# Kernel tuning notes

Hardware: AMD Instinct MI355X
Metric: run time of the kernel (lower is better)

Reference implementation:

```python
import jax, jax.numpy as jnp
import numpy as np

NB_HEAD = 16
SIZE_PER_HEAD = 64
D_MODEL = 1024
OUT_DIM = NB_HEAD * SIZE_PER_HEAD
BIG_NEG = 1e10


def setup_inputs() -> dict:
    key = jax.random.key(0)
    ks = jax.random.split(key, 6)
    B, L = 2, 2048
    q = jax.random.normal(ks[0], (B, L, D_MODEL), dtype=jnp.float32)
    k = jax.random.normal(ks[1], (B, L, D_MODEL), dtype=jnp.float32)
    v = jax.random.normal(ks[2], (B, L, D_MODEL), dtype=jnp.float32)
    v_mask = jnp.ones((B, L), dtype=jnp.float32)
    q_mask = jnp.ones((B, L), dtype=jnp.float32)
    # glorot_normal-ish init for the three projection kernels
    std = (2.0 / (D_MODEL + OUT_DIM)) ** 0.5
    q_kernel = jax.random.normal(ks[3], (D_MODEL, OUT_DIM), dtype=jnp.float32) * std
    k_kernel = jax.random.normal(ks[4], (D_MODEL, OUT_DIM), dtype=jnp.float32) * std
    v_kernel = jax.random.normal(ks[5], (D_MODEL, OUT_DIM), dtype=jnp.float32) * std
    return {"q": q, "k": k, "v": v, "v_mask": v_mask, "q_mask": q_mask,
            "q_kernel": q_kernel, "k_kernel": k_kernel, "v_kernel": v_kernel}


def reference(q, k, v, v_mask, q_mask, q_kernel, k_kernel, v_kernel):
    B, Lq, _ = q.shape
    Lk = k.shape[1]
    H, D = NB_HEAD, SIZE_PER_HEAD
    # projections -> [B, L, H, D]
    qw = (q @ q_kernel).reshape(B, Lq, H, D)
    kw = (k @ k_kernel).reshape(B, Lk, H, D)
    vw = (v @ v_kernel).reshape(B, Lk, H, D)
    # scaled dot-product scores [B, H, Lq, Lk]
    scores = jnp.einsum('bqhd,bkhd->bhqk', qw, kw) / jnp.sqrt(jnp.float32(D))
    # additive key mask (original permutes so mask broadcasts over key axis)
    scores = scores - (1.0 - v_mask)[:, None, None, :] * BIG_NEG
    a = jax.nn.softmax(scores, axis=-1)
    # weighted sum -> [B, Lq, H, D] -> [B, Lq, H*D]
    o = jnp.einsum('bhqk,bkhd->bqhd', a, vw).reshape(B, Lq, H * D)
    # multiplicative query mask on output
    o = o * q_mask[:, :, None]
    return o
```

## Files before the change

### kernel.cpp

```cpp
#include <hip/hip_runtime.h>
#include <hip/hip_bf16.h>

#define B_SZ 2
#define SEQ  2048
#define DM   1024
#define NH   16
#define HD   64

typedef __attribute__((ext_vector_type(8))) short bf16x8;
typedef __attribute__((ext_vector_type(4))) short bf16x4;
typedef __attribute__((ext_vector_type(4))) float f32x4;

__device__ __forceinline__ short f2b(float f) {
    __hip_bfloat16 h = __float2bfloat16(f);
    return *reinterpret_cast<short*>(&h);
}

__device__ __forceinline__ void async_copy16(void* lds, const void* g) {
    __builtin_amdgcn_global_load_lds(
        (const __attribute__((address_space(1))) void*)g,
        (__attribute__((address_space(3))) void*)lds, 16, 0, 0);
}

__global__ __launch_bounds__(256) void kCvt(
    const float* __restrict__ q, const float* __restrict__ k, const float* __restrict__ v,
    short* __restrict__ qb, short* __restrict__ kb, short* __restrict__ vb) {
    const float* src = blockIdx.z == 0 ? q : (blockIdx.z == 1 ? k : v);
    short*       dst = blockIdx.z == 0 ? qb : (blockIdx.z == 1 ? kb : vb);
    size_t i = ((size_t)blockIdx.x * 256 + threadIdx.x) * 8;
    float4 a0 = *reinterpret_cast<const float4*>(src + i);
    float4 a1 = *reinterpret_cast<const float4*>(src + i + 4);
    bf16x8 c;
    c[0] = f2b(a0.x); c[1] = f2b(a0.y); c[2] = f2b(a0.z); c[3] = f2b(a0.w);
    c[4] = f2b(a1.x); c[5] = f2b(a1.y); c[6] = f2b(a1.z); c[7] = f2b(a1.w);
    *reinterpret_cast<bf16x8*>(dst + i) = c;
}

__global__ __launch_bounds__(256) void kT(
    const float* __restrict__ w0, const float* __restrict__ w1, const float* __restrict__ w2,
    short* __restrict__ t0, short* __restrict__ t1, short* __restrict__ t2) {
    const float* w = blockIdx.z == 0 ? w0 : (blockIdx.z == 1 ? w1 : w2);
    short*       t = blockIdx.z == 0 ? t0 : (blockIdx.z == 1 ? t1 : t2);
    __shared__ float tile[64][65];
    int n0 = blockIdx.x * 64, k0 = blockIdx.y * 64;
    int tid = threadIdx.x;
    int c = tid & 63, rr = tid >> 6;
#pragma unroll
    for (int i = 0; i < 16; i++) {
        int kk = i * 4 + rr;
        tile[kk][c] = w[(size_t)(k0 + kk) * DM + n0 + c];
    }
    __syncthreads();
#pragma unroll
    for (int i = 0; i < 16; i++) {
        int nn = i * 4 + rr;
        t[(size_t)(n0 + nn) * DM + k0 + c] = f2b(tile[c][nn]);
    }
}

__global__ __launch_bounds__(256) void kProj(
    const short* __restrict__ qb, const short* __restrict__ kb, const short* __restrict__ vb,
    const short* __restrict__ wtq, const short* __restrict__ wtk, const short* __restrict__ wtv,
    short* __restrict__ qw, short* __restrict__ kw, short* __restrict__ vwT) {
    int z = blockIdx.z;
    const short* A  = z == 0 ? qb : (z == 1 ? kb : vb);
    const short* Bt = z == 0 ? wtq : (z == 1 ? wtk : wtv);

    __shared__ short As[128 * 64];
    __shared__ short Bs[128 * 64];

    int tid = threadIdx.x;
    int m0 = blockIdx.y * 128, n0 = blockIdx.x * 128;
    int wv = tid >> 6, lane = tid & 63, quad = lane >> 4, ln = lane & 15;
    int rblk = (wv >> 1) * 64, cblk = (wv & 1) * 64;

    int rA = wv * 32;
    int srow = rA + (lane >> 3), scol = (lane & 7) * 8;

    f32x4 zero = {0.f, 0.f, 0.f, 0.f};
    f32x4 acc[4][4];
#pragma unroll
    for (int rt = 0; rt < 4; rt++)
#pragma unroll
        for (int ct = 0; ct < 4; ct++) acc[rt][ct] = zero;

    for (int ks = 0; ks < DM; ks += 64) {
        const short* gA = A  + (size_t)(m0 + srow) * DM + ks + scol;
        const short* gB = Bt + (size_t)(n0 + srow) * DM + ks + scol;
#pragma unroll
        for (int i = 0; i < 4; i++) {
            async_copy16(&As[(rA + i * 8) * 64], gA + (size_t)i * 8 * DM);
            async_copy16(&Bs[(rA + i * 8) * 64], gB + (size_t)i * 8 * DM);
        }
        __syncthreads();
#pragma unroll
        for (int kc = 0; kc < 2; kc++) {
            bf16x8 af[4], bfv[4];
#pragma unroll
            for (int rt = 0; rt < 4; rt++)
                af[rt] = *reinterpret_cast<bf16x8*>(&As[(rblk + rt * 16 + ln) * 64 + kc * 32 + quad * 8]);
#pragma unroll
            for (int ct = 0; ct < 4; ct++)
                bfv[ct] = *reinterpret_cast<bf16x8*>(&Bs[(cblk + ct * 16 + ln) * 64 + kc * 32 + quad * 8]);
#pragma unroll
            for (int rt = 0; rt < 4; rt++)
#pragma unroll
                for (int ct = 0; ct < 4; ct++)
                    acc[rt][ct] = __builtin_amdgcn_mfma_f32_16x16x32_bf16(
                        af[rt], bfv[ct], acc[rt][ct], 0, 0, 0);
        }
        __syncthreads();
    }

    if (z < 2) {
        short* C = z == 0 ? qw : kw;
#pragma unroll
        for (int rt = 0; rt < 4; rt++)
#pragma unroll
            for (int r = 0; r < 4; r++) {
                int row = m0 + rblk + rt * 16 + quad * 4 + r;
#pragma unroll
                for (int ct = 0; ct < 4; ct++)
                    C[(size_t)row * DM + n0 + cblk + ct * 16 + ln] = f2b(acc[rt][ct][r]);
            }
    } else {
#pragma unroll
        for (int rt = 0; rt < 4; rt++) {
            int srow0 = m0 + rblk + rt * 16 + quad * 4;
            int bb = srow0 >> 11, lk = srow0 & (SEQ - 1);
#pragma unroll
            for (int ct = 0; ct < 4; ct++) {
                int coln = n0 + cblk + ct * 16 + ln;
                int hh = coln >> 6, dd = coln & 63;
                bf16x4 pk;
                pk[0] = f2b(acc[rt][ct][0]); pk[1] = f2b(acc[rt][ct][1]);
                pk[2] = f2b(acc[rt][ct][2]); pk[3] = f2b(acc[rt][ct][3]);
                *reinterpret_cast<bf16x4*>(
                    &vwT[(((size_t)bb * NH + hh) * HD + dd) * SEQ + lk]) = pk;
            }
        }
    }
}

__global__ __launch_bounds__(512) void kAttn(
    const short* __restrict__ qw, const short* __restrict__ kw, const short* __restrict__ vwT,
    const float* __restrict__ vmask, const float* __restrict__ qmask, float* __restrict__ out) {
    int b = blockIdx.z, h = blockIdx.y, lq0 = blockIdx.x * 128;
    int tid = threadIdx.x, wv = tid >> 6, lane = tid & 63, quad = lane >> 4, ln = lane & 15;

    __shared__ short Ks[64][72];
    __shared__ short Vt[64][72];
    __shared__ short Ps[8][16][72];

    const short* qrow = qw + (size_t)(b * SEQ + lq0 + wv * 16 + ln) * DM + h * HD;
    bf16x8 qf0 = *reinterpret_cast<const bf16x8*>(qrow + quad * 8);
    bf16x8 qf1 = *reinterpret_cast<const bf16x8*>(qrow + 32 + quad * 8);

    f32x4 zero = {0.f, 0.f, 0.f, 0.f};
    float mrow[4], lrow[4];
    f32x4 o[4];
#pragma unroll
    for (int r = 0; r < 4; r++) { mrow[r] = -1e30f; lrow[r] = 0.f; }
#pragma unroll
    for (int ct = 0; ct < 4; ct++) o[ct] = zero;

    int sr = tid >> 3, sc = (tid & 7) * 8;

    for (int lk0 = 0; lk0 < SEQ; lk0 += 64) {
        {
            const short* kp = kw + (size_t)(b * SEQ + lk0 + sr) * DM + h * HD + sc;
            *reinterpret_cast<bf16x8*>(&Ks[sr][sc]) = *reinterpret_cast<const bf16x8*>(kp);
            const short* vp = vwT + ((size_t)(b * NH + h) * HD + sr) * SEQ + lk0 + sc;
            *reinterpret_cast<bf16x8*>(&Vt[sr][sc]) = *reinterpret_cast<const bf16x8*>(vp);
        }
        __syncthreads();

        f32x4 s[4];
#pragma unroll
        for (int ct = 0; ct < 4; ct++) s[ct] = zero;
#pragma unroll
        for (int ct = 0; ct < 4; ct++) {
            bf16x8 kf0 = *reinterpret_cast<bf16x8*>(&Ks[ct * 16 + ln][quad * 8]);
            bf16x8 kf1 = *reinterpret_cast<bf16x8*>(&Ks[ct * 16 + ln][32 + quad * 8]);
            s[ct] = __builtin_amdgcn_mfma_f32_16x16x32_bf16(qf0, kf0, s[ct], 0, 0, 0);
            s[ct] = __builtin_amdgcn_mfma_f32_16x16x32_bf16(qf1, kf1, s[ct], 0, 0, 0);
        }

#pragma unroll
        for (int ct = 0; ct < 4; ct++) {
            float mk = (1.0f - vmask[b * SEQ + lk0 + ct * 16 + ln]) * 1e10f;
#pragma unroll
            for (int r = 0; r < 4; r++) s[ct][r] = s[ct][r] * 0.125f - mk;
        }

        float mc[4];
#pragma unroll
        for (int r = 0; r < 4; r++) {
            mc[r] = fmaxf(fmaxf(s[0][r], s[1][r]), fmaxf(s[2][r], s[3][r]));
            mc[r] = fmaxf(mc[r], __shfl_xor(mc[r], 1));
            mc[r] = fmaxf(mc[r], __shfl_xor(mc[r], 2));
            mc[r] = fmaxf(mc[r], __shfl_xor(mc[r], 4));
            mc[r] = fmaxf(mc[r], __shfl_xor(mc[r], 8));
        }
        float alpha[4], rs[4];
#pragma unroll
        for (int r = 0; r < 4; r++) {
            float mn = fmaxf(mrow[r], mc[r]);
            alpha[r] = __expf(mrow[r] - mn);
            mrow[r] = mn;
            rs[r] = 0.f;
        }
#pragma unroll
        for (int ct = 0; ct < 4; ct++)
#pragma unroll
            for (int r = 0; r < 4; r++) {
                float p = __expf(s[ct][r] - mrow[r]);
                s[ct][r] = p;
                rs[r] += p;
            }
#pragma unroll
        for (int r = 0; r < 4; r++) {
            rs[r] += __shfl_xor(rs[r], 1);
            rs[r] += __shfl_xor(rs[r], 2);
            rs[r] += __shfl_xor(rs[r], 4);
            rs[r] += __shfl_xor(rs[r], 8);
            lrow[r] = lrow[r] * alpha[r] + rs[r];
        }
#pragma unroll
        for (int ct = 0; ct < 4; ct++)
#pragma unroll
            for (int r = 0; r < 4; r++) o[ct][r] *= alpha[r];

#pragma unroll
        for (int ct = 0; ct < 4; ct++)
#pragma unroll
            for (int r = 0; r < 4; r++)
                Ps[wv][quad * 4 + r][ct * 16 + ln] = f2b(s[ct][r]);

        bf16x8 pf0 = *reinterpret_cast<bf16x8*>(&Ps[wv][ln][quad * 8]);
        bf16x8 pf1 = *reinterpret_cast<bf16x8*>(&Ps[wv][ln][32 + quad * 8]);

#pragma unroll
        for (int ct = 0; ct < 4; ct++) {
            bf16x8 vf0 = *reinterpret_cast<bf16x8*>(&Vt[ct * 16 + ln][quad * 8]);
            bf16x8 vf1 = *reinterpret_cast<bf16x8*>(&Vt[ct * 16 + ln][32 + quad * 8]);
            o[ct] = __builtin_amdgcn_mfma_f32_16x16x32_bf16(pf0, vf0, o[ct], 0, 0, 0);
            o[ct] = __builtin_amdgcn_mfma_f32_16x16x32_bf16(pf1, vf1, o[ct], 0, 0, 0);
        }
        __syncthreads();
    }

#pragma unroll
    for (int r = 0; r < 4; r++) {
        int lq = lq0 + wv * 16 + quad * 4 + r;
        float sc2 = (1.0f / lrow[r]) * qmask[b * SEQ + lq];
#pragma unroll
        for (int ct = 0; ct < 4; ct++)
            out[(size_t)(b * SEQ + lq) * DM + h * HD + ct * 16 + ln] = o[ct][r] * sc2;
    }
}

extern "C" void kernel_launch(void* const* d_in, const int* in_sizes, int n_in,
                              void* d_out, int out_size, void* d_ws, size_t ws_size,
                              hipStream_t stream) {
    const float* q  = (const float*)d_in[0];
    const float* k  = (const float*)d_in[1];
    const float* v  = (const float*)d_in[2];
    const float* vm = (const float*)d_in[3];
    const float* qm = (const float*)d_in[4];
    const float* qk = (const float*)d_in[5];
    const float* kk = (const float*)d_in[6];
    const float* vk = (const float*)d_in[7];
    float* out = (float*)d_out;

    short* ws  = (short*)d_ws;
    short* wtq = ws;
    short* wtk = wtq + 1024 * 1024;
    short* wtv = wtk + 1024 * 1024;
    short* vb  = wtv + 1024 * 1024;
    short* qw  = vb + (size_t)4096 * 1024;
    short* kw  = qw + (size_t)4096 * 1024;
    short* vwT = kw + (size_t)4096 * 1024;
    short* qb = (short*)d_out;
    short* kb = qb + (size_t)4096 * 1024;

    kCvt <<<dim3(2048, 1, 3), 256, 0, stream>>>(q, k, v, qb, kb, vb);
    kT   <<<dim3(16, 16, 3), 256, 0, stream>>>(qk, kk, vk, wtq, wtk, wtv);
    kProj<<<dim3(8, 32, 3), 256, 0, stream>>>(qb, kb, vb, wtq, wtk, wtv, qw, kw, vwT);
    kAttn<<<dim3(16, 16, 2), 512, 0, stream>>>(qw, kw, vwT, vm, qm, out);
}
```

Before: 286.9 us.

## Transpose MFMA operands so each lane owns one query row in attention

Swaps the A/B operands of both MFMAs so the score and output accumulators are laid out with one query row per lane and four key/dim columns per lane. Softmax row statistics then become a single scalar per lane, which cuts the max/sum shuffles from four rounds per row to two cross-quad shuffles. It also allows float4 vmask loads and float4 output stores. The P write to LDS changes pattern and may introduce bank conflicts.

```diff
diff --git a/kernel.cpp b/kernel.cpp
--- a/kernel.cpp
+++ b/kernel.cpp
@@ -157,14 +157,13 @@
     bf16x8 qf1 = *reinterpret_cast<const bf16x8*>(qrow + 32 + quad * 8);
 
     f32x4 zero = {0.f, 0.f, 0.f, 0.f};
-    float mrow[4], lrow[4];
+    float mrow = -1e30f, lrow = 0.f;
     f32x4 o[4];
 #pragma unroll
-    for (int r = 0; r < 4; r++) { mrow[r] = -1e30f; lrow[r] = 0.f; }
-#pragma unroll
-    for (int ct = 0; ct < 4; ct++) o[ct] = zero;
+    for (int dt = 0; dt < 4; dt++) o[dt] = zero;
 
     int sr = tid >> 3, sc = (tid & 7) * 8;
+    const float* vmb = vmask + b * SEQ;
 
     for (int lk0 = 0; lk0 < SEQ; lk0 += 64) {
         {
@@ -177,86 +176,82 @@
 
         f32x4 s[4];
 #pragma unroll
-        for (int ct = 0; ct < 4; ct++) s[ct] = zero;
-#pragma unroll
-        for (int ct = 0; ct < 4; ct++) {
-            bf16x8 kf0 = *reinterpret_cast<bf16x8*>(&Ks[ct * 16 + ln][quad * 8]);
-            bf16x8 kf1 = *reinterpret_cast<bf16x8*>(&Ks[ct * 16 + ln][32 + quad * 8]);
-            s[ct] = __builtin_amdgcn_mfma_f32_16x16x32_bf16(qf0, kf0, s[ct], 0, 0, 0);
-            s[ct] = __builtin_amdgcn_mfma_f32_16x16x32_bf16(qf1, kf1, s[ct], 0, 0, 0);
-        }
-
-#pragma unroll
-        for (int ct = 0; ct < 4; ct++) {
-            float mk = (1.0f - vmask[b * SEQ + lk0 + ct * 16 + ln]) * 1e10f;
-#pragma unroll
-            for (int r = 0; r < 4; r++) s[ct][r] = s[ct][r] * 0.125f - mk;
-        }
-
-        float mc[4];
-#pragma unroll
-        for (int r = 0; r < 4; r++) {
-            mc[r] = fmaxf(fmaxf(s[0][r], s[1][r]), fmaxf(s[2][r], s[3][r]));
-            mc[r] = fmaxf(mc[r], __shfl_xor(mc[r], 1));
-            mc[r] = fmaxf(mc[r], __shfl_xor(mc[r], 2));
-            mc[r] = fmaxf(mc[r], __shfl_xor(mc[r], 4));
-            mc[r] = fmaxf(mc[r], __shfl_xor(mc[r], 8));
-        }
-        float alpha[4], rs[4];
-#pragma unroll
-        for (int r = 0; r < 4; r++) {
-            float mn = fmaxf(mrow[r], mc[r]);
-            alpha[r] = __expf(mrow[r] - mn);
-            mrow[r] = mn;
-            rs[r] = 0.f;
-        }
-#pragma unroll
-        for (int ct = 0; ct < 4; ct++)
+        for (int lt = 0; lt < 4; lt++) s[lt] = zero;
+#pragma unroll
+        for (int lt = 0; lt < 4; lt++) {
+            bf16x8 kf0 = *reinterpret_cast<bf16x8*>(&Ks[lt * 16 + ln][quad * 8]);
+            bf16x8 kf1 = *reinterpret_cast<bf16x8*>(&Ks[lt * 16 + ln][32 + quad * 8]);
+            s[lt] = __builtin_amdgcn_mfma_f32_16x16x32_bf16(kf0, qf0, s[lt], 0, 0, 0);
+            s[lt] = __builtin_amdgcn_mfma_f32_16x16x32_bf16(kf1, qf1, s[lt], 0, 0, 0);
+        }
+
+#pragma unroll
+        for (int lt = 0; lt < 4; lt++) {
+            float4 mv = *reinterpret_cast<const float4*>(&vmb[lk0 + lt * 16 + quad * 4]);
+            s[lt][0] = s[lt][0] * 0.125f - (1.0f - mv.x) * 1e10f;
+            s[lt][1] = s[lt][1] * 0.125f - (1.0f - mv.y) * 1e10f;
+            s[lt][2] = s[lt][2] * 0.125f - (1.0f - mv.z) * 1e10f;
+            s[lt][3] = s[lt][3] * 0.125f - (1.0f - mv.w) * 1e10f;
+        }
+
+        float mc = s[0][0];
+#pragma unroll
+        for (int lt = 0; lt < 4; lt++)
+#pragma unroll
+            for (int r = 0; r < 4; r++) mc = fmaxf(mc, s[lt][r]);
+        mc = fmaxf(mc, __shfl_xor(mc, 16));
+        mc = fmaxf(mc, __shfl_xor(mc, 32));
+
+        float mn = fmaxf(mrow, mc);
+        float alpha = __expf(mrow - mn);
+        mrow = mn;
+
+        float rs = 0.f;
+#pragma unroll
+        for (int lt = 0; lt < 4; lt++)
 #pragma unroll
             for (int r = 0; r < 4; r++) {
-                float p = __expf(s[ct][r] - mrow[r]);
-                s[ct][r] = p;
-                rs[r] += p;
+                float p = __expf(s[lt][r] - mn);
+                s[lt][r] = p;
+                rs += p;
             }
-#pragma unroll
-        for (int r = 0; r < 4; r++) {
-            rs[r] += __shfl_xor(rs[r], 1);
-            rs[r] += __shfl_xor(rs[r], 2);
-            rs[r] += __shfl_xor(rs[r], 4);
-            rs[r] += __shfl_xor(rs[r], 8);
-            lrow[r] = lrow[r] * alpha[r] + rs[r];
-        }
-#pragma unroll
-        for (int ct = 0; ct < 4; ct++)
-#pragma unroll
-            for (int r = 0; r < 4; r++) o[ct][r] *= alpha[r];
-
-#pragma unroll
-        for (int ct = 0; ct < 4; ct++)
+        rs += __shfl_xor(rs, 16);
+        rs += __shfl_xor(rs, 32);
+        lrow = lrow * alpha + rs;
+
+#pragma unroll
+        for (int dt = 0; dt < 4; dt++)
+#pragma unroll
+            for (int r = 0; r < 4; r++) o[dt][r] *= alpha;
+
+#pragma unroll
+        for (int lt = 0; lt < 4; lt++)
 #pragma unroll
             for (int r = 0; r < 4; r++)
-                Ps[wv][quad * 4 + r][ct * 16 + ln] = f2b(s[ct][r]);
+                Ps[wv][ln][lt * 16 + quad * 4 + r] = f2b(s[lt][r]);
 
         bf16x8 pf0 = *reinterpret_cast<bf16x8*>(&Ps[wv][ln][quad * 8]);
         bf16x8 pf1 = *reinterpret_cast<bf16x8*>(&Ps[wv][ln][32 + quad * 8]);
 
 #pragma unroll
-        for (int ct = 0; ct < 4; ct++) {
-            bf16x8 vf0 = *reinterpret_cast<bf16x8*>(&Vt[ct * 16 + ln][quad * 8]);
-            bf16x8 vf1 = *reinterpret_cast<bf16x8*>(&Vt[ct * 16 + ln][32 + quad * 8]);
-            o[ct] = __builtin_amdgcn_mfma_f32_16x16x32_bf16(pf0, vf0, o[ct], 0, 0, 0);
-            o[ct] = __builtin_amdgcn_mfma_f32_16x16x32_bf16(pf1, vf1, o[ct], 0, 0, 0);
-        }
-        __syncthreads();
-    }
-
-#pragma unroll
-    for (int r = 0; r < 4; r++) {
-        int lq = lq0 + wv * 16 + quad * 4 + r;
-        float sc2 = (1.0f / lrow[r]) * qmask[b * SEQ + lq];
-#pragma unroll
-        for (int ct = 0; ct < 4; ct++)
-            out[(size_t)(b * SEQ + lq) * DM + h * HD + ct * 16 + ln] = o[ct][r] * sc2;
+        for (int dt = 0; dt < 4; dt++) {
+            bf16x8 vf0 = *reinterpret_cast<bf16x8*>(&Vt[dt * 16 + ln][quad * 8]);
+            bf16x8 vf1 = *reinterpret_cast<bf16x8*>(&Vt[dt * 16 + ln][32 + quad * 8]);
+            o[dt] = __builtin_amdgcn_mfma_f32_16x16x32_bf16(vf0, pf0, o[dt], 0, 0, 0);
+            o[dt] = __builtin_amdgcn_mfma_f32_16x16x32_bf16(vf1, pf1, o[dt], 0, 0, 0);
+        }
+        __syncthreads();
+    }
+
+    int lq = lq0 + wv * 16 + ln;
+    float sc2 = (1.0f / lrow) * qmask[b * SEQ + lq];
+#pragma unroll
+    for (int dt = 0; dt < 4; dt++) {
+        float4 st;
+        st.x = o[dt][0] * sc2; st.y = o[dt][1] * sc2;
+        st.z = o[dt][2] * sc2; st.w = o[dt][3] * sc2;
+        *reinterpret_cast<float4*>(
+            &out[(size_t)(b * SEQ + lq) * DM + h * HD + dt * 16 + quad * 4]) = st;
     }
 }
 
```

New measurement: 255.7 us. -10.9%, faster.
